# Optimization experiments

Measured on AMD Instinct MI355X. Metric: run time of the kernel, lower is better.

Reference implementation:

```python
import jax, jax.numpy as jnp
import numpy as np

N_NODES = 100000
N_EDGES = 3200000
IN_DIM, HID_DIM, LAT_DIM = 128, 64, 64


def gcn_conv(x, edge_index, W, b):
    """PyG-style GCNConv: add self-loops, symmetric deg^-1/2 normalization,
    linear transform, scatter-add aggregation, bias."""
    N = x.shape[0]
    loops = jnp.arange(N, dtype=edge_index.dtype)
    src = jnp.concatenate([edge_index[0], loops])  # [E+N]
    dst = jnp.concatenate([edge_index[1], loops])  # [E+N]
    # degree on target index (with self loops)
    deg = jax.ops.segment_sum(jnp.ones_like(dst, dtype=x.dtype), dst, num_segments=N)
    dinv = jnp.where(deg > 0, jax.lax.rsqrt(deg), 0.0)
    norm = dinv[src] * dinv[dst]  # [E+N]
    h = x @ W  # [N, out_dim] -- transform BEFORE gather (out_dim <= in_dim)
    msg = h[src] * norm[:, None]  # [E+N, out_dim]
    out = jax.ops.segment_sum(msg, dst, num_segments=N)
    return out + b


def setup_inputs() -> dict:
    key = jax.random.key(0)
    ks = jax.random.split(key, 6)
    x = jax.random.normal(ks[0], (N_NODES, IN_DIM), dtype=jnp.float32)
    edge_index = jax.random.randint(ks[1], (2, N_EDGES), 0, N_NODES, dtype=jnp.int64)
    # Glorot-ish init for weights, zero bias (PyG default)
    W1 = jax.random.normal(ks[2], (IN_DIM, HID_DIM), dtype=jnp.float32) / np.sqrt(IN_DIM)
    b1 = jnp.zeros((HID_DIM,), dtype=jnp.float32)
    W2 = jax.random.normal(ks[3], (HID_DIM, LAT_DIM), dtype=jnp.float32) / np.sqrt(HID_DIM)
    b2 = jnp.zeros((LAT_DIM,), dtype=jnp.float32)
    return {"x": x, "edge_index": edge_index, "W1": W1, "b1": b1, "W2": W2, "b2": b2}


def reference(x, edge_index, W1, b1, W2, b2):
    h = jax.nn.relu(gcn_conv(x, edge_index, W1, b1))
    return gcn_conv(h, edge_index, W2, b2)
```

## Files before the change

kernel.cpp:

```cpp
#include <hip/hip_runtime.h>
#include <cstdint>


#define BSHIFT 7
#define NBMAX 784
#define CH 8192
#define MAXB 6016

typedef __attribute__((ext_vector_type(8))) short bf16x8;
typedef __attribute__((ext_vector_type(4))) float f32x4;

__device__ inline unsigned short f2bf(float f) {
    unsigned u = __float_as_uint(f);
    unsigned r = (u + 0x7FFFu + ((u >> 16) & 1u)) >> 16;
    return (unsigned short)r;
}
__device__ inline unsigned pack2(float a, float b) {
    return (unsigned)f2bf(a) | ((unsigned)f2bf(b) << 16);
}
__device__ inline float blo(unsigned u) { return __uint_as_float(u << 16); }
__device__ inline float bhi(unsigned u) { return __uint_as_float(u & 0xFFFF0000u); }

__global__ __launch_bounds__(256) void hist_kernel(const int* __restrict__ dst,
                                                   int* __restrict__ histmat,
                                                   int E, int nb, int nblk,
                                                   const float* __restrict__ W1,
                                                   const float* __restrict__ W2,
                                                   unsigned short* __restrict__ W1t,
                                                   unsigned short* __restrict__ W2t) {
    if (blockIdx.x >= (unsigned)nblk) {
        int i = (blockIdx.x - nblk) * 256 + threadIdx.x;
        if (i < 128 * 64) {
            int k = i >> 6, n = i & 63;
            W1t[n * 128 + k] = f2bf(W1[i]);
        }
        int j = i - 128 * 64;
        if (j >= 0 && j < 64 * 64) {
            int k = j >> 6, n = j & 63;
            W2t[n * 64 + k] = f2bf(W2[j]);
        }
        return;
    }
    __shared__ int hist[NBMAX];
    int t = threadIdx.x;
    for (int b = t; b < nb; b += 256) hist[b] = 0;
    __syncthreads();
    int base = blockIdx.x * CH;
#pragma unroll
    for (int j = 0; j < CH / 1024; ++j) {
        int idx = base + j * 1024 + t * 4;
        if (idx + 4 <= E) {
            int4 d = *(const int4*)(dst + idx);
            atomicAdd(&hist[d.x >> BSHIFT], 1);
            atomicAdd(&hist[d.y >> BSHIFT], 1);
            atomicAdd(&hist[d.z >> BSHIFT], 1);
            atomicAdd(&hist[d.w >> BSHIFT], 1);
        } else {
            for (int k = 0; k < 4; ++k)
                if (idx + k < E) atomicAdd(&hist[dst[idx + k] >> BSHIFT], 1);
        }
    }
    __syncthreads();
    for (int b = t; b < nb; b += 256) histmat[blockIdx.x * nb + b] = hist[b];
}

__global__ __launch_bounds__(256) void scancol_kernel(const int* __restrict__ histmat,
                                                      int* __restrict__ colbase,
                                                      int* __restrict__ buckettotal,
                                                      int nb, int nblk) {
    __shared__ int ts[256];
    int b = blockIdx.x;
    int t = threadIdx.x;
    int v[4];
    int tsum = 0;
#pragma unroll
    for (int k = 0; k < 4; ++k) {
        int blk = t * 4 + k;
        v[k] = (blk < nblk) ? histmat[blk * nb + b] : 0;
        tsum += v[k];
    }
    ts[t] = tsum;
    __syncthreads();
    for (int ofs = 1; ofs < 256; ofs <<= 1) {
        int val = (t >= ofs) ? ts[t - ofs] : 0;
        __syncthreads();
        ts[t] += val;
        __syncthreads();
    }
    int run = ts[t] - tsum;
#pragma unroll
    for (int k = 0; k < 4; ++k) {
        int blk = t * 4 + k;
        if (blk < nblk) colbase[blk * nb + b] = run;
        run += v[k];
    }
    if (t == 255) buckettotal[b] = ts[255];
}

__global__ __launch_bounds__(256) void scanbucket_kernel(const int* __restrict__ buckettotal,
                                                         int* __restrict__ bucketbase,
                                                         int nb, int E) {
    __shared__ int ts[256];
    int t = threadIdx.x;
    int v[4];
    int tsum = 0;
#pragma unroll
    for (int k = 0; k < 4; ++k) {
        int b = t * 4 + k;
        v[k] = (b < nb) ? buckettotal[b] : 0;
        tsum += v[k];
    }
    ts[t] = tsum;
    __syncthreads();
    for (int ofs = 1; ofs < 256; ofs <<= 1) {
        int val = (t >= ofs) ? ts[t - ofs] : 0;
        __syncthreads();
        ts[t] += val;
        __syncthreads();
    }
    int run = ts[t] - tsum;
#pragma unroll
    for (int k = 0; k < 4; ++k) {
        int b = t * 4 + k;
        if (b < nb) bucketbase[b] = run;
        run += v[k];
    }
    if (t == 0) bucketbase[nb] = E;
}

__global__ __launch_bounds__(256) void bscatter_kernel(const int* __restrict__ src,
                                                       const int* __restrict__ dst,
                                                       const int* __restrict__ colbase,
                                                       const int* __restrict__ bucketbase,
                                                       int* __restrict__ packed,
                                                       int E, int nb) {
    __shared__ int cur[NBMAX];
    int t = threadIdx.x;
    for (int b = t; b < nb; b += 256)
        cur[b] = bucketbase[b] + colbase[blockIdx.x * nb + b];
    __syncthreads();
    int base = blockIdx.x * CH;
#pragma unroll
    for (int j = 0; j < CH / 1024; ++j) {
        int idx = base + j * 1024 + t * 4;
        if (idx + 4 <= E) {
            int4 d = *(const int4*)(dst + idx);
            int4 s = *(const int4*)(src + idx);
            int p;
            p = atomicAdd(&cur[d.x >> BSHIFT], 1); packed[p] = ((d.x & 127) << 17) | s.x;
            p = atomicAdd(&cur[d.y >> BSHIFT], 1); packed[p] = ((d.y & 127) << 17) | s.y;
            p = atomicAdd(&cur[d.z >> BSHIFT], 1); packed[p] = ((d.z & 127) << 17) | s.z;
            p = atomicAdd(&cur[d.w >> BSHIFT], 1); packed[p] = ((d.w & 127) << 17) | s.w;
        } else {
            for (int k = 0; k < 4; ++k)
                if (idx + k < E) {
                    int dd = dst[idx + k], ss = src[idx + k];
                    int p = atomicAdd(&cur[dd >> BSHIFT], 1);
                    packed[p] = ((dd & 127) << 17) | ss;
                }
        }
    }
}

__global__ __launch_bounds__(256) void bcsr_kernel(const int* __restrict__ packed,
                                                   const int* __restrict__ bucketbase,
                                                   int* __restrict__ rowptr,
                                                   float* __restrict__ dinv,
                                                   int* __restrict__ csr,
                                                   int N, int nb) {
    __shared__ int deg[128];
    __shared__ int lrp[128];
    __shared__ int ts[128];
    __shared__ int ebuf[MAXB];
    __shared__ int obuf[MAXB];
    int b = blockIdx.x;
    int t = threadIdx.x;
    if (t < 128) deg[t] = 0;
    __syncthreads();
    int bb0 = bucketbase[b];
    int bb1 = bucketbase[b + 1];
    int cnt = bb1 - bb0;
    bool fits = (cnt <= MAXB);
    if (fits) {
        for (int i = t; i < cnt; i += 256) {
            int v = packed[bb0 + i];
            ebuf[i] = v;
            atomicAdd(&deg[v >> 17], 1);
        }
    } else {
        for (int i = t; i < cnt; i += 256)
            atomicAdd(&deg[packed[bb0 + i] >> 17], 1);
    }
    __syncthreads();
    if (t < 128) ts[t] = deg[t];
    __syncthreads();
    for (int ofs = 1; ofs < 128; ofs <<= 1) {
        int v = (t < 128 && t >= ofs) ? ts[t - ofs] : 0;
        __syncthreads();
        if (t < 128) ts[t] += v;
        __syncthreads();
    }
    int node0 = b << BSHIFT;
    int nlocal = min(128, N - node0);
    if (t < 128) lrp[t] = ts[t] - deg[t];
    if (t < nlocal) {
        rowptr[node0 + t] = bb0 + (ts[t] - deg[t]);
        dinv[node0 + t] = rsqrtf((float)(deg[t] + 1));
    }
    if (t == nlocal) rowptr[node0 + nlocal] = bb1;
    __syncthreads();
    if (fits) {
        for (int i = t; i < cnt; i += 256) {
            int v = ebuf[i];
            int p = atomicAdd(&lrp[v >> 17], 1);
            obuf[p] = v & 0x1FFFF;
        }
        __syncthreads();
        for (int i = t; i < cnt; i += 256) csr[bb0 + i] = obuf[i];
    } else {
        for (int i = t; i < cnt; i += 256) {
            int v = packed[bb0 + i];
            int p = atomicAdd(&lrp[v >> 17], 1);
            csr[bb0 + p] = v & 0x1FFFF;
        }
    }
}

template <int K, bool XBF16>
__global__ __launch_bounds__(256) void gemm_mfma(const void* __restrict__ Xv,
                                                 const unsigned short* __restrict__ Wt,
                                                 const float* __restrict__ dinv,
                                                 unsigned short* __restrict__ Ybf, int M) {
    constexpr int KP = K + 8;
    __shared__ unsigned short Xs[64 * KP];
    __shared__ unsigned short Ws[64 * KP];
    int t = threadIdx.x;
    int row0 = blockIdx.x * 64;

    for (int i = t; i < 64 * K / 8; i += 256) {
        int r = i / (K / 8), c8 = i % (K / 8);
        *(uint4*)(&Ws[r * KP + c8 * 8]) = ((const uint4*)Wt)[i];
    }
    if (XBF16) {
        const unsigned short* X = (const unsigned short*)Xv;
        for (int i = t; i < 64 * K / 8; i += 256) {
            int r = i / (K / 8), c8 = i % (K / 8);
            int gr = row0 + r;
            uint4 v = make_uint4(0u, 0u, 0u, 0u);
            if (gr < M) v = ((const uint4*)(X + (size_t)gr * K))[c8];
            *(uint4*)(&Xs[r * KP + c8 * 8]) = v;
        }
    } else {
        const float* X = (const float*)Xv;
        for (int i = t; i < 64 * K / 4; i += 256) {
            int r = i / (K / 4), c4 = i % (K / 4);
            int gr = row0 + r;
            float4 v = make_float4(0.f, 0.f, 0.f, 0.f);
            if (gr < M) v = ((const float4*)(X + (size_t)gr * K))[c4];
            uint2 p;
            p.x = pack2(v.x, v.y);
            p.y = pack2(v.z, v.w);
            *(uint2*)(&Xs[r * KP + c4 * 4]) = p;
        }
    }
    __syncthreads();

    int lane = t & 63;
    int w = t >> 6;
    int m = lane & 15;
    int q = lane >> 4;

    f32x4 acc[4];
#pragma unroll
    for (int nt = 0; nt < 4; ++nt) acc[nt] = (f32x4){0.f, 0.f, 0.f, 0.f};

#pragma unroll
    for (int s = 0; s < K / 32; ++s) {
        bf16x8 a = *(const bf16x8*)(&Xs[(16 * w + m) * KP + s * 32 + q * 8]);
#pragma unroll
        for (int nt = 0; nt < 4; ++nt) {
            bf16x8 b = *(const bf16x8*)(&Ws[(16 * nt + m) * KP + s * 32 + q * 8]);
            acc[nt] = __builtin_amdgcn_mfma_f32_16x16x32_bf16(a, b, acc[nt], 0, 0, 0);
        }
    }
    __syncthreads();

    unsigned short* Cs = Xs;
#pragma unroll
    for (int nt = 0; nt < 4; ++nt)
#pragma unroll
        for (int r = 0; r < 4; ++r) {
            int row = 16 * w + q * 4 + r;
            int gr = row0 + row;
            float d = (gr < M) ? dinv[gr] : 0.f;
            Cs[row * 72 + nt * 16 + m] = f2bf(acc[nt][r] * d);
        }
    __syncthreads();
    for (int i = t; i < 64 * 64 / 8; i += 256) {
        int r = i >> 3, c8 = i & 7;
        int gr = row0 + r;
        if (gr < M)
            *(uint4*)(Ybf + (size_t)gr * 64 + c8 * 8) = *(const uint4*)(&Cs[r * 72 + c8 * 8]);
    }
}

#define ACC8(v)                                      \
    acc[0] += blo(v.x); acc[1] += bhi(v.x);          \
    acc[2] += blo(v.y); acc[3] += bhi(v.y);          \
    acc[4] += blo(v.z); acc[5] += bhi(v.z);          \
    acc[6] += blo(v.w); acc[7] += bhi(v.w);

__global__ __launch_bounds__(256) void aggregate_kernel(const unsigned* __restrict__ hsu,
                                                        const int* __restrict__ rowptr,
                                                        const int* __restrict__ csr,
                                                        const float* __restrict__ dinv,
                                                        const float* __restrict__ bias,
                                                        void* __restrict__ outv, int N,
                                                        int do_relu, int obf) {
    int t = threadIdx.x;
    int node = blockIdx.x * 32 + (t >> 3);
    if (node >= N) return;
    int sub = t & 7;
    int gbase = t & 56;

    float acc[8];
    {
        uint4 v = *(const uint4*)(hsu + (size_t)node * 32 + sub * 4);
        acc[0] = blo(v.x); acc[1] = bhi(v.x);
        acc[2] = blo(v.y); acc[3] = bhi(v.y);
        acc[4] = blo(v.z); acc[5] = bhi(v.z);
        acc[6] = blo(v.w); acc[7] = bhi(v.w);
    }
    int e0 = rowptr[node];
    int e1 = rowptr[node + 1];

    int e = e0;
    for (; e + 8 <= e1; e += 8) {
        int idx = csr[e + sub];
        int s0 = __shfl(idx, gbase + 0, 64);
        int s1 = __shfl(idx, gbase + 1, 64);
        int s2 = __shfl(idx, gbase + 2, 64);
        int s3 = __shfl(idx, gbase + 3, 64);
        int s4 = __shfl(idx, gbase + 4, 64);
        int s5 = __shfl(idx, gbase + 5, 64);
        int s6 = __shfl(idx, gbase + 6, 64);
        int s7 = __shfl(idx, gbase + 7, 64);
        uint4 v0 = *(const uint4*)(hsu + (size_t)s0 * 32 + sub * 4);
        uint4 v1 = *(const uint4*)(hsu + (size_t)s1 * 32 + sub * 4);
        uint4 v2 = *(const uint4*)(hsu + (size_t)s2 * 32 + sub * 4);
        uint4 v3 = *(const uint4*)(hsu + (size_t)s3 * 32 + sub * 4);
        uint4 v4 = *(const uint4*)(hsu + (size_t)s4 * 32 + sub * 4);
        uint4 v5 = *(const uint4*)(hsu + (size_t)s5 * 32 + sub * 4);
        uint4 v6 = *(const uint4*)(hsu + (size_t)s6 * 32 + sub * 4);
        uint4 v7 = *(const uint4*)(hsu + (size_t)s7 * 32 + sub * 4);
        ACC8(v0); ACC8(v1); ACC8(v2); ACC8(v3);
        ACC8(v4); ACC8(v5); ACC8(v6); ACC8(v7);
    }
    for (; e < e1; ++e) {
        int s = csr[e];
        uint4 v = *(const uint4*)(hsu + (size_t)s * 32 + sub * 4);
        ACC8(v);
    }

    float d = dinv[node];
    float4 b0 = *(const float4*)(bias + sub * 8);
    float4 b1 = *(const float4*)(bias + sub * 8 + 4);
    float o[8];
    o[0] = fmaf(acc[0], d, b0.x); o[1] = fmaf(acc[1], d, b0.y);
    o[2] = fmaf(acc[2], d, b0.z); o[3] = fmaf(acc[3], d, b0.w);
    o[4] = fmaf(acc[4], d, b1.x); o[5] = fmaf(acc[5], d, b1.y);
    o[6] = fmaf(acc[6], d, b1.z); o[7] = fmaf(acc[7], d, b1.w);
    if (do_relu) {
#pragma unroll
        for (int k = 0; k < 8; ++k) o[k] = fmaxf(o[k], 0.f);
    }
    if (obf) {
        unsigned short* outb = (unsigned short*)outv;
        uint4 p;
        p.x = pack2(o[0], o[1]); p.y = pack2(o[2], o[3]);
        p.z = pack2(o[4], o[5]); p.w = pack2(o[6], o[7]);
        *(uint4*)(outb + (size_t)node * 64 + sub * 8) = p;
    } else {
        float* op = (float*)outv + (size_t)node * 64 + sub * 8;
        *(float4*)(op)     = make_float4(o[0], o[1], o[2], o[3]);
        *(float4*)(op + 4) = make_float4(o[4], o[5], o[6], o[7]);
    }
}

extern "C" void kernel_launch(void* const* d_in, const int* in_sizes, int n_in,
                              void* d_out, int out_size, void* d_ws, size_t ws_size,
                              hipStream_t stream) {
    const float* x  = (const float*)d_in[0];
    const int*   ei = (const int*)d_in[1];
    const float* W1 = (const float*)d_in[2];
    const float* b1 = (const float*)d_in[3];
    const float* W2 = (const float*)d_in[4];
    const float* b2 = (const float*)d_in[5];

    const int N = in_sizes[0] / 128;
    const int E = in_sizes[1] / 2;
    const int* src = ei;
    const int* dst = ei + E;
    float* out = (float*)d_out;

    const int nb   = (N + 127) >> BSHIFT;
    const int nblk = (E + CH - 1) / CH;

    char* ws = (char*)d_ws;
    size_t off = 0;
    auto alloc = [&](size_t bytes) -> char* {
        char* p = ws + off;
        off = (off + bytes + 255) & ~(size_t)255;
        return p;
    };
    int*   csr         = (int*)alloc((size_t)E * 4);
    int*   rowptr      = (int*)alloc((size_t)(N + 1) * 4);
    float* dinv        = (float*)alloc((size_t)N * 4);
    int*   bucketbase  = (int*)alloc((size_t)(nb + 1) * 4);
    int*   buckettotal = (int*)alloc((size_t)nb * 4);
    unsigned short* W1t = (unsigned short*)alloc(64 * 128 * 2);
    unsigned short* W2t = (unsigned short*)alloc(64 * 64 * 2);
    unsigned short* bufA = (unsigned short*)alloc((size_t)N * 64 * 2);
    unsigned short* bufB = (unsigned short*)alloc((size_t)N * 64 * 2);
    int* histmat = (int*)bufA;
    int* packed  = (int*)((char*)bufA + ((size_t)nblk * nb * 4 + 255 & ~(size_t)255) + 256);

    hist_kernel<<<nblk + 48, 256, 0, stream>>>(dst, histmat, E, nb, nblk, W1, W2, W1t, W2t);
    scancol_kernel<<<nb, 256, 0, stream>>>(histmat, histmat, buckettotal, nb, nblk);
    scanbucket_kernel<<<1, 256, 0, stream>>>(buckettotal, bucketbase, nb, E);
    bscatter_kernel<<<nblk, 256, 0, stream>>>(src, dst, histmat, bucketbase, packed, E, nb);
    bcsr_kernel<<<nb, 256, 0, stream>>>(packed, bucketbase, rowptr, dinv, csr, N, nb);

    gemm_mfma<128, false><<<(N + 63) / 64, 256, 0, stream>>>(x, W1t, dinv, bufA, N);
    aggregate_kernel<<<(N + 31) / 32, 256, 0, stream>>>((const unsigned*)bufA, rowptr, csr,
                                                        dinv, b1, bufB, N, 1, 1);
    gemm_mfma<64, true><<<(N + 63) / 64, 256, 0, stream>>>(bufB, W2t, dinv, bufA, N);
    aggregate_kernel<<<(N + 31) / 32, 256, 0, stream>>>((const unsigned*)bufA, rowptr, csr,
                                                        dinv, b2, out, N, 0, 0);
}
```

Baseline: 320.1 us.

## Fuse layer-2 GEMM into first aggregation and fold bucket scan into consumers

The first aggregation kernel now applies bias and ReLU, stages its 32-node tile in LDS, and multiplies it by W2 with MFMA before writing the dinv-scaled bf16 result. This removes the separate layer-2 GEMM launch and its read and write of the hidden buffer. The single-block bucket scan kernel is also removed: each bscatter and bcsr block recomputes the bucket prefix sum from the bucket totals. That saves a launch and a serialization point, but every block now repeats the scan, and the fused kernel uses more LDS and adds barriers.

Result: faster. 310.2 us (-3.1%).

```diff
diff --git a/kernel.cpp b/kernel.cpp
--- a/kernel.cpp
+++ b/kernel.cpp
@@ -97,47 +97,38 @@
     if (t == 255) buckettotal[b] = ts[255];
 }
 
-__global__ __launch_bounds__(256) void scanbucket_kernel(const int* __restrict__ buckettotal,
-                                                         int* __restrict__ bucketbase,
-                                                         int nb, int E) {
-    __shared__ int ts[256];
-    int t = threadIdx.x;
-    int v[4];
-    int tsum = 0;
-#pragma unroll
-    for (int k = 0; k < 4; ++k) {
-        int b = t * 4 + k;
-        v[k] = (b < nb) ? buckettotal[b] : 0;
-        tsum += v[k];
-    }
-    ts[t] = tsum;
-    __syncthreads();
-    for (int ofs = 1; ofs < 256; ofs <<= 1) {
-        int val = (t >= ofs) ? ts[t - ofs] : 0;
-        __syncthreads();
-        ts[t] += val;
-        __syncthreads();
-    }
-    int run = ts[t] - tsum;
-#pragma unroll
-    for (int k = 0; k < 4; ++k) {
-        int b = t * 4 + k;
-        if (b < nb) bucketbase[b] = run;
-        run += v[k];
-    }
-    if (t == 0) bucketbase[nb] = E;
-}
-
 __global__ __launch_bounds__(256) void bscatter_kernel(const int* __restrict__ src,
                                                        const int* __restrict__ dst,
                                                        const int* __restrict__ colbase,
-                                                       const int* __restrict__ bucketbase,
+                                                       const int* __restrict__ buckettotal,
                                                        int* __restrict__ packed,
                                                        int E, int nb) {
     __shared__ int cur[NBMAX];
+    __shared__ int ts2[256];
     int t = threadIdx.x;
-    for (int b = t; b < nb; b += 256)
-        cur[b] = bucketbase[b] + colbase[blockIdx.x * nb + b];
+    int v4[4];
+    int tsum = 0;
+#pragma unroll
+    for (int k = 0; k < 4; ++k) {
+        int bb = t * 4 + k;
+        v4[k] = (bb < nb) ? buckettotal[bb] : 0;
+        tsum += v4[k];
+    }
+    ts2[t] = tsum;
+    __syncthreads();
+    for (int ofs = 1; ofs < 256; ofs <<= 1) {
+        int val = (t >= ofs) ? ts2[t - ofs] : 0;
+        __syncthreads();
+        ts2[t] += val;
+        __syncthreads();
+    }
+    int run = ts2[t] - tsum;
+#pragma unroll
+    for (int k = 0; k < 4; ++k) {
+        int bb = t * 4 + k;
+        if (bb < nb) cur[bb] = run + colbase[blockIdx.x * nb + bb];
+        run += v4[k];
+    }
     __syncthreads();
     int base = blockIdx.x * CH;
 #pragma unroll
@@ -163,7 +154,7 @@
 }
 
 __global__ __launch_bounds__(256) void bcsr_kernel(const int* __restrict__ packed,
-                                                   const int* __restrict__ bucketbase,
+                                                   const int* __restrict__ buckettotal,
                                                    int* __restrict__ rowptr,
                                                    float* __restrict__ dinv,
                                                    int* __restrict__ csr,
@@ -171,14 +162,39 @@
     __shared__ int deg[128];
     __shared__ int lrp[128];
     __shared__ int ts[128];
+    __shared__ int ts2[256];
+    __shared__ int shbb[2];
     __shared__ int ebuf[MAXB];
     __shared__ int obuf[MAXB];
     int b = blockIdx.x;
     int t = threadIdx.x;
     if (t < 128) deg[t] = 0;
-    __syncthreads();
-    int bb0 = bucketbase[b];
-    int bb1 = bucketbase[b + 1];
+    int v4[4];
+    int tsum = 0;
+#pragma unroll
+    for (int k = 0; k < 4; ++k) {
+        int bb = t * 4 + k;
+        v4[k] = (bb < nb) ? buckettotal[bb] : 0;
+        tsum += v4[k];
+    }
+    ts2[t] = tsum;
+    __syncthreads();
+    for (int ofs = 1; ofs < 256; ofs <<= 1) {
+        int val = (t >= ofs) ? ts2[t - ofs] : 0;
+        __syncthreads();
+        ts2[t] += val;
+        __syncthreads();
+    }
+    int run = ts2[t] - tsum;
+#pragma unroll
+    for (int k = 0; k < 4; ++k) {
+        int bb = t * 4 + k;
+        if (bb == b) { shbb[0] = run; shbb[1] = run + v4[k]; }
+        run += v4[k];
+    }
+    __syncthreads();
+    int bb0 = shbb[0];
+    int bb1 = shbb[1];
     int cnt = bb1 - bb0;
     bool fits = (cnt <= MAXB);
     if (fits) {
@@ -310,77 +326,131 @@
     acc[4] += blo(v.z); acc[5] += bhi(v.z);          \
     acc[6] += blo(v.w); acc[7] += bhi(v.w);
 
+template <bool DO_GEMM>
 __global__ __launch_bounds__(256) void aggregate_kernel(const unsigned* __restrict__ hsu,
                                                         const int* __restrict__ rowptr,
                                                         const int* __restrict__ csr,
                                                         const float* __restrict__ dinv,
                                                         const float* __restrict__ bias,
-                                                        void* __restrict__ outv, int N,
-                                                        int do_relu, int obf) {
+                                                        const unsigned short* __restrict__ W2t,
+                                                        void* __restrict__ outv, int N) {
+    __shared__ unsigned short Hs[DO_GEMM ? 32 * 72 : 1];
+    __shared__ unsigned short W2s[DO_GEMM ? 64 * 72 : 1];
+    __shared__ unsigned short Cs[DO_GEMM ? 32 * 72 : 1];
     int t = threadIdx.x;
-    int node = blockIdx.x * 32 + (t >> 3);
-    if (node >= N) return;
+    int node0 = blockIdx.x * 32;
+    int node = node0 + (t >> 3);
     int sub = t & 7;
     int gbase = t & 56;
 
-    float acc[8];
-    {
-        uint4 v = *(const uint4*)(hsu + (size_t)node * 32 + sub * 4);
-        acc[0] = blo(v.x); acc[1] = bhi(v.x);
-        acc[2] = blo(v.y); acc[3] = bhi(v.y);
-        acc[4] = blo(v.z); acc[5] = bhi(v.z);
-        acc[6] = blo(v.w); acc[7] = bhi(v.w);
-    }
-    int e0 = rowptr[node];
-    int e1 = rowptr[node + 1];
-
-    int e = e0;
-    for (; e + 8 <= e1; e += 8) {
-        int idx = csr[e + sub];
-        int s0 = __shfl(idx, gbase + 0, 64);
-        int s1 = __shfl(idx, gbase + 1, 64);
-        int s2 = __shfl(idx, gbase + 2, 64);
-        int s3 = __shfl(idx, gbase + 3, 64);
-        int s4 = __shfl(idx, gbase + 4, 64);
-        int s5 = __shfl(idx, gbase + 5, 64);
-        int s6 = __shfl(idx, gbase + 6, 64);
-        int s7 = __shfl(idx, gbase + 7, 64);
-        uint4 v0 = *(const uint4*)(hsu + (size_t)s0 * 32 + sub * 4);
-        uint4 v1 = *(const uint4*)(hsu + (size_t)s1 * 32 + sub * 4);
-        uint4 v2 = *(const uint4*)(hsu + (size_t)s2 * 32 + sub * 4);
-        uint4 v3 = *(const uint4*)(hsu + (size_t)s3 * 32 + sub * 4);
-        uint4 v4 = *(const uint4*)(hsu + (size_t)s4 * 32 + sub * 4);
-        uint4 v5 = *(const uint4*)(hsu + (size_t)s5 * 32 + sub * 4);
-        uint4 v6 = *(const uint4*)(hsu + (size_t)s6 * 32 + sub * 4);
-        uint4 v7 = *(const uint4*)(hsu + (size_t)s7 * 32 + sub * 4);
-        ACC8(v0); ACC8(v1); ACC8(v2); ACC8(v3);
-        ACC8(v4); ACC8(v5); ACC8(v6); ACC8(v7);
-    }
-    for (; e < e1; ++e) {
-        int s = csr[e];
-        uint4 v = *(const uint4*)(hsu + (size_t)s * 32 + sub * 4);
-        ACC8(v);
-    }
-
-    float d = dinv[node];
-    float4 b0 = *(const float4*)(bias + sub * 8);
-    float4 b1 = *(const float4*)(bias + sub * 8 + 4);
-    float o[8];
-    o[0] = fmaf(acc[0], d, b0.x); o[1] = fmaf(acc[1], d, b0.y);
-    o[2] = fmaf(acc[2], d, b0.z); o[3] = fmaf(acc[3], d, b0.w);
-    o[4] = fmaf(acc[4], d, b1.x); o[5] = fmaf(acc[5], d, b1.y);
-    o[6] = fmaf(acc[6], d, b1.z); o[7] = fmaf(acc[7], d, b1.w);
-    if (do_relu) {
-#pragma unroll
-        for (int k = 0; k < 8; ++k) o[k] = fmaxf(o[k], 0.f);
-    }
-    if (obf) {
+    if (DO_GEMM) {
+        for (int i = t; i < 64 * 64 / 8; i += 256) {
+            int r = i >> 3, c8 = i & 7;
+            *(uint4*)(&W2s[r * 72 + c8 * 8]) = ((const uint4*)W2t)[i];
+        }
+    }
+
+    float acc[8] = {0.f, 0.f, 0.f, 0.f, 0.f, 0.f, 0.f, 0.f};
+    if (node < N) {
+        {
+            uint4 v = *(const uint4*)(hsu + (size_t)node * 32 + sub * 4);
+            acc[0] = blo(v.x); acc[1] = bhi(v.x);
+            acc[2] = blo(v.y); acc[3] = bhi(v.y);
+            acc[4] = blo(v.z); acc[5] = bhi(v.z);
+            acc[6] = blo(v.w); acc[7] = bhi(v.w);
+        }
+        int e0 = rowptr[node];
+        int e1 = rowptr[node + 1];
+        int e = e0;
+        for (; e + 8 <= e1; e += 8) {
+            int idx = csr[e + sub];
+            int s0 = __shfl(idx, gbase + 0, 64);
+            int s1 = __shfl(idx, gbase + 1, 64);
+            int s2 = __shfl(idx, gbase + 2, 64);
+            int s3 = __shfl(idx, gbase + 3, 64);
+            int s4 = __shfl(idx, gbase + 4, 64);
+            int s5 = __shfl(idx, gbase + 5, 64);
+            int s6 = __shfl(idx, gbase + 6, 64);
+            int s7 = __shfl(idx, gbase + 7, 64);
+            uint4 v0 = *(const uint4*)(hsu + (size_t)s0 * 32 + sub * 4);
+            uint4 v1 = *(const uint4*)(hsu + (size_t)s1 * 32 + sub * 4);
+            uint4 v2 = *(const uint4*)(hsu + (size_t)s2 * 32 + sub * 4);
+            uint4 v3 = *(const uint4*)(hsu + (size_t)s3 * 32 + sub * 4);
+            uint4 v4 = *(const uint4*)(hsu + (size_t)s4 * 32 + sub * 4);
+            uint4 v5 = *(const uint4*)(hsu + (size_t)s5 * 32 + sub * 4);
+            uint4 v6 = *(const uint4*)(hsu + (size_t)s6 * 32 + sub * 4);
+            uint4 v7 = *(const uint4*)(hsu + (size_t)s7 * 32 + sub * 4);
+            ACC8(v0); ACC8(v1); ACC8(v2); ACC8(v3);
+            ACC8(v4); ACC8(v5); ACC8(v6); ACC8(v7);
+        }
+        for (; e < e1; ++e) {
+            int s = csr[e];
+            uint4 v = *(const uint4*)(hsu + (size_t)s * 32 + sub * 4);
+            ACC8(v);
+        }
+    }
+
+    if (DO_GEMM) {
+        if (node < N) {
+            float d = dinv[node];
+            float4 b0 = *(const float4*)(bias + sub * 8);
+            float4 b1 = *(const float4*)(bias + sub * 8 + 4);
+            float o[8];
+            o[0] = fmaxf(fmaf(acc[0], d, b0.x), 0.f);
+            o[1] = fmaxf(fmaf(acc[1], d, b0.y), 0.f);
+            o[2] = fmaxf(fmaf(acc[2], d, b0.z), 0.f);
+            o[3] = fmaxf(fmaf(acc[3], d, b0.w), 0.f);
+            o[4] = fmaxf(fmaf(acc[4], d, b1.x), 0.f);
+            o[5] = fmaxf(fmaf(acc[5], d, b1.y), 0.f);
+            o[6] = fmaxf(fmaf(acc[6], d, b1.z), 0.f);
+            o[7] = fmaxf(fmaf(acc[7], d, b1.w), 0.f);
+            uint4 p;
+            p.x = pack2(o[0], o[1]); p.y = pack2(o[2], o[3]);
+            p.z = pack2(o[4], o[5]); p.w = pack2(o[6], o[7]);
+            *(uint4*)(&Hs[(t >> 3) * 72 + sub * 8]) = p;
+        }
+        __syncthreads();
+        int lane = t & 63;
+        int w = t >> 6;
+        int m = lane & 15;
+        int q = lane >> 4;
+        int mt = w & 1;
+#pragma unroll
+        for (int half = 0; half < 2; ++half) {
+            int nt = (w >> 1) + half * 2;
+            f32x4 a4 = (f32x4){0.f, 0.f, 0.f, 0.f};
+#pragma unroll
+            for (int s = 0; s < 2; ++s) {
+                bf16x8 a = *(const bf16x8*)(&Hs[(mt * 16 + m) * 72 + s * 32 + q * 8]);
+                bf16x8 b = *(const bf16x8*)(&W2s[(nt * 16 + m) * 72 + s * 32 + q * 8]);
+                a4 = __builtin_amdgcn_mfma_f32_16x16x32_bf16(a, b, a4, 0, 0, 0);
+            }
+#pragma unroll
+            for (int r = 0; r < 4; ++r) {
+                int row = mt * 16 + q * 4 + r;
+                int gn = node0 + row;
+                float dd = (gn < N) ? dinv[gn] : 0.f;
+                Cs[row * 72 + nt * 16 + m] = f2bf(a4[r] * dd);
+            }
+        }
+        __syncthreads();
         unsigned short* outb = (unsigned short*)outv;
-        uint4 p;
-        p.x = pack2(o[0], o[1]); p.y = pack2(o[2], o[3]);
-        p.z = pack2(o[4], o[5]); p.w = pack2(o[6], o[7]);
-        *(uint4*)(outb + (size_t)node * 64 + sub * 8) = p;
+        for (int i = t; i < 32 * 64 / 8; i += 256) {
+            int r = i >> 3, c8 = i & 7;
+            int gn = node0 + r;
+            if (gn < N)
+                *(uint4*)(outb + (size_t)gn * 64 + c8 * 8) = *(const uint4*)(&Cs[r * 72 + c8 * 8]);
+        }
     } else {
+        if (node >= N) return;
+        float d = dinv[node];
+        float4 b0 = *(const float4*)(bias + sub * 8);
+        float4 b1 = *(const float4*)(bias + sub * 8 + 4);
+        float o[8];
+        o[0] = fmaf(acc[0], d, b0.x); o[1] = fmaf(acc[1], d, b0.y);
+        o[2] = fmaf(acc[2], d, b0.z); o[3] = fmaf(acc[3], d, b0.w);
+        o[4] = fmaf(acc[4], d, b1.x); o[5] = fmaf(acc[5], d, b1.y);
+        o[6] = fmaf(acc[6], d, b1.z); o[7] = fmaf(acc[7], d, b1.w);
         float* op = (float*)outv + (size_t)node * 64 + sub * 8;
         *(float4*)(op)     = make_float4(o[0], o[1], o[2], o[3]);
         *(float4*)(op + 4) = make_float4(o[4], o[5], o[6], o[7]);
@@ -416,7 +486,6 @@
     int*   csr         = (int*)alloc((size_t)E * 4);
     int*   rowptr      = (int*)alloc((size_t)(N + 1) * 4);
     float* dinv        = (float*)alloc((size_t)N * 4);
-    int*   bucketbase  = (int*)alloc((size_t)(nb + 1) * 4);
     int*   buckettotal = (int*)alloc((size_t)nb * 4);
     unsigned short* W1t = (unsigned short*)alloc(64 * 128 * 2);
     unsigned short* W2t = (unsigned short*)alloc(64 * 64 * 2);
@@ -427,14 +496,12 @@
 
     hist_kernel<<<nblk + 48, 256, 0, stream>>>(dst, histmat, E, nb, nblk, W1, W2, W1t, W2t);
     scancol_kernel<<<nb, 256, 0, stream>>>(histmat, histmat, buckettotal, nb, nblk);
-    scanbucket_kernel<<<1, 256, 0, stream>>>(buckettotal, bucketbase, nb, E);
-    bscatter_kernel<<<nblk, 256, 0, stream>>>(src, dst, histmat, bucketbase, packed, E, nb);
-    bcsr_kernel<<<nb, 256, 0, stream>>>(packed, bucketbase, rowptr, dinv, csr, N, nb);
+    bscatter_kernel<<<nblk, 256, 0, stream>>>(src, dst, histmat, buckettotal, packed, E, nb);
+    bcsr_kernel<<<nb, 256, 0, stream>>>(packed, buckettotal, rowptr, dinv, csr, N, nb);
 
     gemm_mfma<128, false><<<(N + 63) / 64, 256, 0, stream>>>(x, W1t, dinv, bufA, N);
-    aggregate_kernel<<<(N + 31) / 32, 256, 0, stream>>>((const unsigned*)bufA, rowptr, csr,
-                                                        dinv, b1, bufB, N, 1, 1);
-    gemm_mfma<64, true><<<(N + 63) / 64, 256, 0, stream>>>(bufB, W2t, dinv, bufA, N);
-    aggregate_kernel<<<(N + 31) / 32, 256, 0, stream>>>((const unsigned*)bufA, rowptr, csr,
-                                                        dinv, b2, out, N, 0, 0);
-}
+    aggregate_kernel<true><<<(N + 31) / 32, 256, 0, stream>>>((const unsigned*)bufA, rowptr,
+                                                              csr, dinv, b1, W2t, bufB, N);
+    aggregate_kernel<false><<<(N + 31) / 32, 256, 0, stream>>>((const unsigned*)bufB, rowptr,
+                                                               csr, dinv, b2, W2t, out, N);
+}
```
